# Performance work log

Measured on AMD Instinct MI355X. Metric: run time of the kernel, lower is better.

The kernel has to match this reference:

```python
import jax, jax.numpy as jnp
import numpy as np

LAM = 5.0
NUM_STEPS = 100
B, N, D = 8, 1024, 256


def setup_inputs() -> dict:
    key = jax.random.key(0)
    k1, k2 = jax.random.split(key)
    fA = jax.random.normal(k1, (B, N, D), dtype=jnp.float32)
    fB = jax.random.normal(k2, (B, N, D), dtype=jnp.float32)
    dustbin = jnp.zeros((1,), dtype=jnp.float32)  # learned dustbin score, init 0.0
    return {"fA": fA, "fB": fB, "dustbin": dustbin}


def _l2_normalize(x, eps=1e-12):
    # matches tf.math.l2_normalize: x / sqrt(max(sum(x^2), eps))
    return x * jax.lax.rsqrt(jnp.maximum(jnp.sum(x * x, axis=-1, keepdims=True), eps))


def _forward(fA, fB, dustbin):
    b, n, _ = fA.shape
    fA = _l2_normalize(fA)
    fB = _l2_normalize(fB)
    Sij = jnp.einsum('bnd,bmd->bnm', fA, fB)  # (B, N, N)
    # augment with dustbin row/col -> (B, N+1, N+1)
    row = dustbin * jnp.ones((b, 1, n), Sij.dtype)
    col = dustbin * jnp.ones((b, n + 1, 1), Sij.dtype)
    S_aug = jnp.concatenate([jnp.concatenate([Sij, row], axis=1), col], axis=2)
    Cij = jnp.clip(-S_aug, -15.0 / LAM, 15.0 / LAM)
    # marginals: [1,...,1, N] for both rows and cols
    ab = jnp.concatenate([jnp.ones((n,), Sij.dtype), jnp.full((1,), float(n), Sij.dtype)])[None, :]  # (1, N+1)
    P = jnp.exp(-LAM * Cij)
    P = P / jnp.sum(P, axis=(1, 2), keepdims=True)

    def step(P, _):
        # NOTE: row_sum/col_sum both computed from the SAME P, as in the TF code
        row_sum = jnp.sum(P, axis=1)  # (B, N+1)
        col_sum = jnp.sum(P, axis=2)  # (B, N+1)
        P = P * (ab / col_sum)[:, :, None]
        P = P * (ab / row_sum)[:, None, :]
        return P, None

    P, _ = jax.lax.scan(jax.checkpoint(step), P, None, length=NUM_STEPS)
    return P


def reference(fA, fB, dustbin):
    return _forward(fA, fB, dustbin)
```

## Files before the change

### kernel.cpp

```cpp
#include <hip/hip_runtime.h>
#include <math.h>
#include <stdint.h>

#define NB 8
#define NN 1024
#define DD 256
#define NP1 1025
#define LDP 1028
#define NSTEPS 100

__global__ __launch_bounds__(256) void norm_kernel(const float* __restrict__ fA,
                                                   const float* __restrict__ fB,
                                                   float* __restrict__ invA,
                                                   float* __restrict__ invB) {
  int gw = (blockIdx.x * 256 + threadIdx.x) >> 6;
  int lane = threadIdx.x & 63;
  const float* src;
  float* dst;
  int row;
  if (gw < NB * NN) { src = fA; dst = invA; row = gw; }
  else              { src = fB; dst = invB; row = gw - NB * NN; }
  float4 v = *(const float4*)(src + (size_t)row * DD + lane * 4);
  double ss = (double)v.x * v.x + (double)v.y * v.y + (double)v.z * v.z + (double)v.w * v.w;
#pragma unroll
  for (int o = 32; o; o >>= 1) ss += __shfl_xor(ss, o, 64);
  if (lane == 0) dst[row] = (float)(1.0 / sqrt(fmax(ss, 1e-12)));
}

__global__ __launch_bounds__(256) void gemm_exp_kernel(const float* __restrict__ fA,
                                                       const float* __restrict__ fB,
                                                       const float* __restrict__ invA,
                                                       const float* __restrict__ invB,
                                                       float* __restrict__ P0,
                                                       double* __restrict__ partZ) {
  const int id = blockIdx.x;
  const int b = id & 7;
  const int tile = id >> 3;
  const int bx = tile & 15, by = tile >> 4;
  const int row0 = by * 64, col0 = bx * 64;
  const int tid = threadIdx.x;
  const int tx = tid & 15, ty = tid >> 4;
  __shared__ __align__(16) float As[16][68];
  __shared__ __align__(16) float Bs[16][68];
  __shared__ double zred[256];
  float acc[4][4] = {{0.f}};
  const int lm = tid >> 2, kq = (tid & 3) << 2;
  const float sa = invA[b * NN + row0 + lm];
  const float sb = invB[b * NN + col0 + lm];
  const float* pA = fA + (size_t)(b * NN + row0 + lm) * DD + kq;
  const float* pB = fB + (size_t)(b * NN + col0 + lm) * DD + kq;
  for (int k0 = 0; k0 < DD; k0 += 16) {
    const float4 a4 = *(const float4*)(pA + k0);
    const float4 b4 = *(const float4*)(pB + k0);
    As[kq + 0][lm] = a4.x * sa; As[kq + 1][lm] = a4.y * sa;
    As[kq + 2][lm] = a4.z * sa; As[kq + 3][lm] = a4.w * sa;
    Bs[kq + 0][lm] = b4.x * sb; Bs[kq + 1][lm] = b4.y * sb;
    Bs[kq + 2][lm] = b4.z * sb; Bs[kq + 3][lm] = b4.w * sb;
    __syncthreads();
#pragma unroll
    for (int kk = 0; kk < 16; ++kk) {
      const float4 av = *(const float4*)&As[kk][ty * 4];
      const float4 bv = *(const float4*)&Bs[kk][tx * 4];
      const float ar[4] = {av.x, av.y, av.z, av.w};
      const float br[4] = {bv.x, bv.y, bv.z, bv.w};
#pragma unroll
      for (int a = 0; a < 4; ++a)
#pragma unroll
        for (int e = 0; e < 4; ++e)
          acc[a][e] = fmaf(ar[a], br[e], acc[a][e]);
    }
    __syncthreads();
  }
  double zs = 0.0;
#pragma unroll
  for (int a = 0; a < 4; ++a)
#pragma unroll
    for (int e = 0; e < 4; ++e) {
      const float S = acc[a][e];
      const float C = fminf(fmaxf(-S, -3.0f), 3.0f);
      const float p = expf(-5.0f * C);
      acc[a][e] = p;
      zs += (double)p;
    }
  {
    float* P0b = P0 + (size_t)b * NP1 * LDP;
#pragma unroll
    for (int a = 0; a < 4; ++a) {
      float4 v;
      v.x = acc[a][0]; v.y = acc[a][1]; v.z = acc[a][2]; v.w = acc[a][3];
      *(float4*)(P0b + (size_t)(row0 + ty * 4 + a) * LDP + col0 + tx * 4) = v;
    }
  }
  zred[tid] = zs;
  __syncthreads();
#pragma unroll
  for (int o = 128; o; o >>= 1) {
    if (tid < o) zred[tid] += zred[tid + o];
    __syncthreads();
  }
  if (tid == 0) partZ[(b * 16 + by) * 16 + bx] = zred[0];
}

__global__ __launch_bounds__(1024) void fill_dustbin_kernel(const float* __restrict__ dustbin,
                                                            float* __restrict__ P0) {
  const int b = blockIdx.x, tid = threadIdx.x;
  const float d = dustbin[0];
  const float dv = expf(-5.0f * fminf(fmaxf(-d, -3.0f), 3.0f));
  float* P0b = P0 + (size_t)b * NP1 * LDP;
  for (int j = tid; j < NP1; j += 1024) {
    P0b[(size_t)NN * LDP + j] = dv;
    P0b[(size_t)j * LDP + NN] = dv;
  }
}

__global__ __launch_bounds__(256) void init_rc_kernel(const double* __restrict__ partZ,
                                                      float* __restrict__ r0,
                                                      double* __restrict__ Binit,
                                                      double* __restrict__ Bzero) {
  const int b = blockIdx.x, tid = threadIdx.x;
  __shared__ double red[256];
  red[tid] = partZ[b * 256 + tid];
  __syncthreads();
#pragma unroll
  for (int o = 128; o; o >>= 1) {
    if (tid < o) red[tid] += red[tid + o];
    __syncthreads();
  }
  const double Z = red[0];
  const float rv = (float)(1.0 / Z);
  for (int i = tid; i < NP1; i += 256) {
    r0[b * NP1 + i] = rv;
    Binit[b * NP1 + i] = (i == NN) ? (double)NN : 1.0;
    Bzero[b * NP1 + i] = 0.0;
  }
}

__global__ __launch_bounds__(512, 4) void step_kernel(const float* __restrict__ P0,
                                                      const float* __restrict__ rin,
                                                      float* __restrict__ rout,
                                                      const double* __restrict__ Bprev,
                                                      double* __restrict__ Bacc,
                                                      double* __restrict__ Bzero) {
  const int id = blockIdx.x;
  const int b = id & 7;
  const int s = id >> 3;
  const int tid = threadIdx.x;
  const int lane = tid & 63;
  const int wv = tid >> 6;

  __shared__ __align__(16) double c_lds[NP1 + 3];
  __shared__ __align__(16) float part_lds[8][LDP];

  const float* P0b = P0 + (size_t)b * NP1 * LDP;
  const float* rv_in = rin + b * NP1;
  const int rowA = s * 16 + wv;
  const int rowB = rowA + 8;
  const bool special = (s == 63 && wv == 7);
  const float wA = rv_in[rowA];
  const float wB = rv_in[rowB];
  const float4* pA4 = (const float4*)(P0b + (size_t)rowA * LDP);
  const float4* pB4 = (const float4*)(P0b + (size_t)rowB * LDP);
  const float4* pC4 = (const float4*)(P0b + (size_t)NN * LDP);

  float4 a4[4], b4[4];
#pragma unroll
  for (int k = 0; k < 4; ++k) {
    a4[k] = pA4[lane + (k << 6)];
    b4[k] = pB4[lane + (k << 6)];
  }
  float aT = 0.f, bT = 0.f;
  if (lane == 0) {
    aT = ((const float*)pA4)[NN];
    bT = ((const float*)pB4)[NN];
  }
  float4 c4[4];
  float cT = 0.f, wC = 0.f;
  if (special) {
#pragma unroll
    for (int k = 0; k < 4; ++k) c4[k] = pC4[lane + (k << 6)];
    if (lane == 0) cT = ((const float*)pC4)[NN];
    wC = rv_in[NN];
  }

  if (tid < 17) {
    const int idx = id * 17 + tid;
    if (idx < NB * NP1) Bzero[idx] = 0.0;
  }
  const double* Bp = Bprev + b * NP1;
  for (int j = tid; j < NP1; j += 512)
    c_lds[j] = ((j == NN) ? (double)NN : 1.0) / Bp[j];
  __syncthreads();

  double dotA = 0.0, dotB = 0.0, dotC = 0.0;
  float4 part[4];
#pragma unroll
  for (int k = 0; k < 4; ++k) {
    const int j4 = lane + (k << 6);
    const double2 c01 = *(const double2*)&c_lds[4 * j4];
    const double2 c23 = *(const double2*)&c_lds[4 * j4 + 2];
    dotA += (double)a4[k].x * c01.x + (double)a4[k].y * c01.y +
            (double)a4[k].z * c23.x + (double)a4[k].w * c23.y;
    dotB += (double)b4[k].x * c01.x + (double)b4[k].y * c01.y +
            (double)b4[k].z * c23.x + (double)b4[k].w * c23.y;
    part[k].x = fmaf(wA, a4[k].x, wB * b4[k].x);
    part[k].y = fmaf(wA, a4[k].y, wB * b4[k].y);
    part[k].z = fmaf(wA, a4[k].z, wB * b4[k].z);
    part[k].w = fmaf(wA, a4[k].w, wB * b4[k].w);
    if (special) {
      dotC += (double)c4[k].x * c01.x + (double)c4[k].y * c01.y +
              (double)c4[k].z * c23.x + (double)c4[k].w * c23.y;
      part[k].x = fmaf(wC, c4[k].x, part[k].x);
      part[k].y = fmaf(wC, c4[k].y, part[k].y);
      part[k].z = fmaf(wC, c4[k].z, part[k].z);
      part[k].w = fmaf(wC, c4[k].w, part[k].w);
    }
  }
  float ptail = 0.f;
  if (lane == 0) {
    const double cN = c_lds[NN];
    dotA += (double)aT * cN;
    dotB += (double)bT * cN;
    ptail = wA * aT + wB * bT;
    if (special) { dotC += (double)cT * cN; ptail = fmaf(wC, cT, ptail); }
  }
#pragma unroll
  for (int o = 32; o; o >>= 1) {
    dotA += __shfl_xor(dotA, o, 64);
    dotB += __shfl_xor(dotB, o, 64);
  }
  if (special) {
#pragma unroll
    for (int o = 32; o; o >>= 1) dotC += __shfl_xor(dotC, o, 64);
  }
  if (lane == 0) {
    float* ro = rout + b * NP1;
    ro[rowA] = (float)(1.0 / dotA);
    ro[rowB] = (float)(1.0 / dotB);
    if (special) ro[NN] = (float)((double)NN / dotC);
  }
  {
    float4* pl4 = (float4*)&part_lds[wv][0];
#pragma unroll
    for (int k = 0; k < 4; ++k) pl4[lane + (k << 6)] = part[k];
    if (lane == 0) part_lds[wv][NN] = ptail;
  }
  __syncthreads();
  double* Ba = Bacc + b * NP1;
  for (int j = tid; j < NP1; j += 512) {
    const float s0 = ((part_lds[0][j] + part_lds[1][j]) + (part_lds[2][j] + part_lds[3][j])) +
                     ((part_lds[4][j] + part_lds[5][j]) + (part_lds[6][j] + part_lds[7][j]));
    atomicAdd(Ba + j, (double)s0);
  }
}

__global__ __launch_bounds__(256) void cfinal_kernel(const double* __restrict__ Bfin,
                                                     float* __restrict__ cfin) {
  const int b = blockIdx.x;
  for (int j = threadIdx.x; j < NP1; j += 256)
    cfin[b * LDP + j] = (float)(((j == NN) ? (double)NN : 1.0) / Bfin[b * NP1 + j]);
}

__global__ __launch_bounds__(256) void finalize_kernel(const float* __restrict__ P0,
                                                       float* __restrict__ Pout,
                                                       const float* __restrict__ rfin,
                                                       const float* __restrict__ cfin) {
  const int bi = blockIdx.x;
  const int b = bi & 7, i = bi >> 3;
  const int tid = threadIdx.x;
  const float rv = rfin[b * NP1 + i];
  const float4* src = (const float4*)(P0 + (size_t)b * NP1 * LDP + (size_t)i * LDP);
  const float4* cv = (const float4*)(cfin + b * LDP);
  float* dst = Pout + (size_t)b * NP1 * NP1 + (size_t)i * NP1;
  const float4 p = src[tid];
  const float4 c = cv[tid];
  dst[tid * 4 + 0] = rv * p.x * c.x;
  dst[tid * 4 + 1] = rv * p.y * c.y;
  dst[tid * 4 + 2] = rv * p.z * c.z;
  dst[tid * 4 + 3] = rv * p.w * c.w;
  if (tid == 0)
    dst[NN] = rv * ((const float*)src)[NN] * cfin[b * LDP + NN];
}

extern "C" void kernel_launch(void* const* d_in, const int* in_sizes, int n_in,
                              void* d_out, int out_size, void* d_ws, size_t ws_size,
                              hipStream_t stream) {
  const float* fA = (const float*)d_in[0];
  const float* fB = (const float*)d_in[1];
  const float* dustbin = (const float*)d_in[2];

  float* Pout = (float*)d_out;

  float* P0 = (float*)d_ws;
  float* rbuf = P0 + (size_t)NB * NP1 * LDP;
  float* cfin = rbuf + 2 * NB * NP1;
  double* Bbuf = (double*)(((uintptr_t)(cfin + NB * LDP) + 15) & ~(uintptr_t)15);
  double* partZ = Bbuf + 3 * NB * NP1;
  float* invA = (float*)(partZ + NB * 256);
  float* invB = invA + NB * NN;

  norm_kernel<<<4096, 256, 0, stream>>>(fA, fB, invA, invB);
  gemm_exp_kernel<<<2048, 256, 0, stream>>>(fA, fB, invA, invB, P0, partZ);
  fill_dustbin_kernel<<<NB, 1024, 0, stream>>>(dustbin, P0);
  init_rc_kernel<<<NB, 256, 0, stream>>>(partZ, rbuf, Bbuf + 2 * NB * NP1, Bbuf);

  for (int t = 0; t < NSTEPS; ++t) {
    float* rin = rbuf + (t & 1) * NB * NP1;
    float* rout = rbuf + ((t + 1) & 1) * NB * NP1;
    double* Bprev = Bbuf + ((t + 2) % 3) * NB * NP1;
    double* Bacc = Bbuf + (t % 3) * NB * NP1;
    double* Bzero = Bbuf + ((t + 1) % 3) * NB * NP1;
    step_kernel<<<512, 512, 0, stream>>>(P0, rin, rout, Bprev, Bacc, Bzero);
  }

  cfinal_kernel<<<NB, 256, 0, stream>>>(Bbuf, cfin);
  finalize_kernel<<<NB * NP1, 256, 0, stream>>>(P0, Pout, rbuf, cfin);
}
```

Before: 967.6 us.

## Replace per-step launches with a persistent cooperative Sinkhorn kernel caching P0 in LDS

```diff
diff --git a/kernel.cpp b/kernel.cpp
--- a/kernel.cpp
+++ b/kernel.cpp
@@ -113,10 +113,10 @@
   }
 }
 
-__global__ __launch_bounds__(256) void init_rc_kernel(const double* __restrict__ partZ,
-                                                      float* __restrict__ r0,
-                                                      double* __restrict__ Binit,
-                                                      double* __restrict__ Bzero) {
+__global__ __launch_bounds__(256) void init2_kernel(const double* __restrict__ partZ,
+                                                    float* __restrict__ rinit,
+                                                    double* __restrict__ B0,
+                                                    unsigned* __restrict__ ctr) {
   const int b = blockIdx.x, tid = threadIdx.x;
   __shared__ double red[256];
   red[tid] = partZ[b * 256 + tid];
@@ -126,131 +126,161 @@
     if (tid < o) red[tid] += red[tid + o];
     __syncthreads();
   }
-  const double Z = red[0];
-  const float rv = (float)(1.0 / Z);
-  for (int i = tid; i < NP1; i += 256) {
-    r0[b * NP1 + i] = rv;
-    Binit[b * NP1 + i] = (i == NN) ? (double)NN : 1.0;
-    Bzero[b * NP1 + i] = 0.0;
-  }
-}
-
-__global__ __launch_bounds__(512, 4) void step_kernel(const float* __restrict__ P0,
-                                                      const float* __restrict__ rin,
-                                                      float* __restrict__ rout,
-                                                      const double* __restrict__ Bprev,
-                                                      double* __restrict__ Bacc,
-                                                      double* __restrict__ Bzero) {
+  if (tid == 0) rinit[b] = (float)(1.0 / red[0]);
+  for (int j = tid; j < NP1; j += 256) B0[b * NP1 + j] = 0.0;
+  for (int t = tid; t < NSTEPS; t += 256) ctr[t * 8 + b] = 0u;
+}
+
+__global__ __launch_bounds__(512) void sinkhorn_persist(const float* __restrict__ P0,
+                                                        const float* __restrict__ dustbin,
+                                                        const float* __restrict__ rinit,
+                                                        double* __restrict__ Bbuf,
+                                                        unsigned* __restrict__ ctr,
+                                                        float* __restrict__ rfin) {
+  __shared__ __align__(16) float P0s[32][LDP];
+  __shared__ __align__(16) float c_f[LDP];
+  __shared__ __align__(16) float part[LDP];
+  __shared__ double wred[8];
+  __shared__ float rN_sh;
+
   const int id = blockIdx.x;
   const int b = id & 7;
   const int s = id >> 3;
   const int tid = threadIdx.x;
   const int lane = tid & 63;
   const int wv = tid >> 6;
-
-  __shared__ __align__(16) double c_lds[NP1 + 3];
-  __shared__ __align__(16) float part_lds[8][LDP];
-
-  const float* P0b = P0 + (size_t)b * NP1 * LDP;
-  const float* rv_in = rin + b * NP1;
-  const int rowA = s * 16 + wv;
-  const int rowB = rowA + 8;
-  const bool special = (s == 63 && wv == 7);
-  const float wA = rv_in[rowA];
-  const float wB = rv_in[rowB];
-  const float4* pA4 = (const float4*)(P0b + (size_t)rowA * LDP);
-  const float4* pB4 = (const float4*)(P0b + (size_t)rowB * LDP);
-  const float4* pC4 = (const float4*)(P0b + (size_t)NN * LDP);
-
-  float4 a4[4], b4[4];
-#pragma unroll
-  for (int k = 0; k < 4; ++k) {
-    a4[k] = pA4[lane + (k << 6)];
-    b4[k] = pB4[lane + (k << 6)];
-  }
-  float aT = 0.f, bT = 0.f;
+  const int row0 = s * 32;
+  const int wrow = wv * 4;
+  const bool desig = (s == 31);
+
+  const float d = dustbin[0];
+  const float dv = expf(-5.0f * fminf(fmaxf(-d, -3.0f), 3.0f));
+
+  {
+    const float4* src = (const float4*)(P0 + ((size_t)b * NP1 + row0) * LDP);
+    float4* dst = (float4*)&P0s[0][0];
+    for (int idx = tid; idx < 32 * (LDP / 4); idx += 512) dst[idx] = src[idx];
+  }
+  const float rv0 = rinit[b];
+  float r4[4] = {rv0, rv0, rv0, rv0};
+  if (tid == 0) rN_sh = rv0;
+  __syncthreads();
+
+  for (int t = 0; t < NSTEPS; ++t) {
+    double* Bacc = Bbuf + (size_t)(t % 3) * NB * NP1 + (size_t)b * NP1;
+    if (t == 0) {
+      for (int j = tid; j < LDP; j += 512) c_f[j] = 1.0f;
+    } else {
+      double* Bp = Bbuf + (size_t)((t + 2) % 3) * NB * NP1 + (size_t)b * NP1;
+      for (int j = tid; j < NP1; j += 512) {
+        const double bj = __hip_atomic_load(&Bp[j], __ATOMIC_RELAXED, __HIP_MEMORY_SCOPE_AGENT);
+        c_f[j] = (float)(((j == NN) ? (double)NN : 1.0) / bj);
+      }
+      if (tid < 3) c_f[NP1 + tid] = 0.0f;
+    }
+    {
+      double cs = (t == 0) ? ((tid == 0) ? 3.0 : 2.0)
+                           : (double)c_f[tid] + (double)c_f[tid + 512] +
+                             ((tid == 0) ? (double)c_f[1024] : 0.0);
+#pragma unroll
+      for (int o = 32; o; o >>= 1) cs += __shfl_xor(cs, o, 64);
+      if (lane == 0) wred[wv] = cs;
+    }
+    {
+      double* Bz = Bbuf + (size_t)((t + 1) % 3) * NB * NP1 + (size_t)b * NP1;
+      if (tid < 33) {
+        const int j = s * 33 + tid;
+        if (j < NP1) __hip_atomic_store(&Bz[j], 0.0, __ATOMIC_RELAXED, __HIP_MEMORY_SCOPE_AGENT);
+      }
+    }
+    {
+      const float pinit = desig ? rN_sh * dv : 0.0f;
+      for (int j = tid; j < LDP; j += 512) part[j] = pinit;
+    }
+    __syncthreads();
+
+    const float cN = c_f[NN];
+    double dot0 = 0.0, dot1 = 0.0, dot2 = 0.0, dot3 = 0.0;
+    float4 pacc[4];
+#pragma unroll
+    for (int k = 0; k < 4; ++k) { pacc[k].x = 0.f; pacc[k].y = 0.f; pacc[k].z = 0.f; pacc[k].w = 0.f; }
+#pragma unroll
+    for (int k = 0; k < 4; ++k) {
+      const int j4 = (lane << 2) + (k << 8);
+      const float4 cc = *(const float4*)&c_f[j4];
+      const double c0 = cc.x, c1 = cc.y, c2 = cc.z, c3 = cc.w;
+#pragma unroll
+      for (int q = 0; q < 4; ++q) {
+        const float4 v = *(const float4*)&P0s[wrow + q][j4];
+        const double dd = (double)v.x * c0 + (double)v.y * c1 +
+                          (double)v.z * c2 + (double)v.w * c3;
+        if (q == 0) dot0 += dd; else if (q == 1) dot1 += dd;
+        else if (q == 2) dot2 += dd; else dot3 += dd;
+        pacc[k].x = fmaf(r4[q], v.x, pacc[k].x);
+        pacc[k].y = fmaf(r4[q], v.y, pacc[k].y);
+        pacc[k].z = fmaf(r4[q], v.z, pacc[k].z);
+        pacc[k].w = fmaf(r4[q], v.w, pacc[k].w);
+      }
+    }
+    float ptail = 0.f;
+    if (lane == 0) {
+#pragma unroll
+      for (int q = 0; q < 4; ++q) {
+        const float vN = P0s[wrow + q][NN];
+        const double dd = (double)vN * (double)cN;
+        if (q == 0) dot0 += dd; else if (q == 1) dot1 += dd;
+        else if (q == 2) dot2 += dd; else dot3 += dd;
+        ptail = fmaf(r4[q], vN, ptail);
+      }
+    }
+#pragma unroll
+    for (int o = 32; o; o >>= 1) {
+      dot0 += __shfl_xor(dot0, o, 64);
+      dot1 += __shfl_xor(dot1, o, 64);
+      dot2 += __shfl_xor(dot2, o, 64);
+      dot3 += __shfl_xor(dot3, o, 64);
+    }
+    r4[0] = (float)(1.0 / dot0);
+    r4[1] = (float)(1.0 / dot1);
+    r4[2] = (float)(1.0 / dot2);
+    r4[3] = (float)(1.0 / dot3);
+#pragma unroll
+    for (int k = 0; k < 4; ++k) {
+      const int j4 = (lane << 2) + (k << 8);
+      atomicAdd(&part[j4 + 0], pacc[k].x);
+      atomicAdd(&part[j4 + 1], pacc[k].y);
+      atomicAdd(&part[j4 + 2], pacc[k].z);
+      atomicAdd(&part[j4 + 3], pacc[k].w);
+    }
+    if (lane == 0) atomicAdd(&part[NN], ptail);
+    if (desig && tid == 0) {
+      const double sumc = ((wred[0] + wred[1]) + (wred[2] + wred[3])) +
+                          ((wred[4] + wred[5]) + (wred[6] + wred[7]));
+      rN_sh = (float)((double)NN / ((double)dv * sumc));
+    }
+    __syncthreads();
+    for (int j = tid; j < NP1; j += 512)
+      atomicAdd(&Bacc[j], (double)part[j]);
+    if (t < NSTEPS - 1) {
+      __syncthreads();
+      if (tid == 0) {
+        __hip_atomic_fetch_add(&ctr[t * 8 + b], 1u, __ATOMIC_RELEASE, __HIP_MEMORY_SCOPE_AGENT);
+        unsigned v = 0; int guard = 0;
+        do {
+          v = __hip_atomic_load(&ctr[t * 8 + b], __ATOMIC_ACQUIRE, __HIP_MEMORY_SCOPE_AGENT);
+          if (v >= 32u) break;
+          __builtin_amdgcn_s_sleep(1);
+        } while (++guard < (1 << 20));
+      }
+      __syncthreads();
+    }
+  }
   if (lane == 0) {
-    aT = ((const float*)pA4)[NN];
-    bT = ((const float*)pB4)[NN];
-  }
-  float4 c4[4];
-  float cT = 0.f, wC = 0.f;
-  if (special) {
-#pragma unroll
-    for (int k = 0; k < 4; ++k) c4[k] = pC4[lane + (k << 6)];
-    if (lane == 0) cT = ((const float*)pC4)[NN];
-    wC = rv_in[NN];
-  }
-
-  if (tid < 17) {
-    const int idx = id * 17 + tid;
-    if (idx < NB * NP1) Bzero[idx] = 0.0;
-  }
-  const double* Bp = Bprev + b * NP1;
-  for (int j = tid; j < NP1; j += 512)
-    c_lds[j] = ((j == NN) ? (double)NN : 1.0) / Bp[j];
-  __syncthreads();
-
-  double dotA = 0.0, dotB = 0.0, dotC = 0.0;
-  float4 part[4];
-#pragma unroll
-  for (int k = 0; k < 4; ++k) {
-    const int j4 = lane + (k << 6);
-    const double2 c01 = *(const double2*)&c_lds[4 * j4];
-    const double2 c23 = *(const double2*)&c_lds[4 * j4 + 2];
-    dotA += (double)a4[k].x * c01.x + (double)a4[k].y * c01.y +
-            (double)a4[k].z * c23.x + (double)a4[k].w * c23.y;
-    dotB += (double)b4[k].x * c01.x + (double)b4[k].y * c01.y +
-            (double)b4[k].z * c23.x + (double)b4[k].w * c23.y;
-    part[k].x = fmaf(wA, a4[k].x, wB * b4[k].x);
-    part[k].y = fmaf(wA, a4[k].y, wB * b4[k].y);
-    part[k].z = fmaf(wA, a4[k].z, wB * b4[k].z);
-    part[k].w = fmaf(wA, a4[k].w, wB * b4[k].w);
-    if (special) {
-      dotC += (double)c4[k].x * c01.x + (double)c4[k].y * c01.y +
-              (double)c4[k].z * c23.x + (double)c4[k].w * c23.y;
-      part[k].x = fmaf(wC, c4[k].x, part[k].x);
-      part[k].y = fmaf(wC, c4[k].y, part[k].y);
-      part[k].z = fmaf(wC, c4[k].z, part[k].z);
-      part[k].w = fmaf(wC, c4[k].w, part[k].w);
-    }
-  }
-  float ptail = 0.f;
-  if (lane == 0) {
-    const double cN = c_lds[NN];
-    dotA += (double)aT * cN;
-    dotB += (double)bT * cN;
-    ptail = wA * aT + wB * bT;
-    if (special) { dotC += (double)cT * cN; ptail = fmaf(wC, cT, ptail); }
-  }
-#pragma unroll
-  for (int o = 32; o; o >>= 1) {
-    dotA += __shfl_xor(dotA, o, 64);
-    dotB += __shfl_xor(dotB, o, 64);
-  }
-  if (special) {
-#pragma unroll
-    for (int o = 32; o; o >>= 1) dotC += __shfl_xor(dotC, o, 64);
-  }
-  if (lane == 0) {
-    float* ro = rout + b * NP1;
-    ro[rowA] = (float)(1.0 / dotA);
-    ro[rowB] = (float)(1.0 / dotB);
-    if (special) ro[NN] = (float)((double)NN / dotC);
-  }
-  {
-    float4* pl4 = (float4*)&part_lds[wv][0];
-#pragma unroll
-    for (int k = 0; k < 4; ++k) pl4[lane + (k << 6)] = part[k];
-    if (lane == 0) part_lds[wv][NN] = ptail;
-  }
-  __syncthreads();
-  double* Ba = Bacc + b * NP1;
-  for (int j = tid; j < NP1; j += 512) {
-    const float s0 = ((part_lds[0][j] + part_lds[1][j]) + (part_lds[2][j] + part_lds[3][j])) +
-                     ((part_lds[4][j] + part_lds[5][j]) + (part_lds[6][j] + part_lds[7][j]));
-    atomicAdd(Ba + j, (double)s0);
-  }
+    float* ro = rfin + b * NP1;
+#pragma unroll
+    for (int q = 0; q < 4; ++q) ro[row0 + wrow + q] = r4[q];
+  }
+  if (desig && tid == 0) rfin[b * NP1 + NN] = rN_sh;
 }
 
 __global__ __launch_bounds__(256) void cfinal_kernel(const double* __restrict__ Bfin,
@@ -291,27 +321,25 @@
   float* Pout = (float*)d_out;
 
   float* P0 = (float*)d_ws;
-  float* rbuf = P0 + (size_t)NB * NP1 * LDP;
-  float* cfin = rbuf + 2 * NB * NP1;
+  float* rfin = P0 + (size_t)NB * NP1 * LDP;
+  float* cfin = rfin + NB * NP1;
   double* Bbuf = (double*)(((uintptr_t)(cfin + NB * LDP) + 15) & ~(uintptr_t)15);
   double* partZ = Bbuf + 3 * NB * NP1;
-  float* invA = (float*)(partZ + NB * 256);
+  float* rinit = (float*)(partZ + NB * 256);
+  unsigned* ctr = (unsigned*)(rinit + 8);
+  float* invA = (float*)(ctr + NSTEPS * 8);
   float* invB = invA + NB * NN;
 
   norm_kernel<<<4096, 256, 0, stream>>>(fA, fB, invA, invB);
   gemm_exp_kernel<<<2048, 256, 0, stream>>>(fA, fB, invA, invB, P0, partZ);
   fill_dustbin_kernel<<<NB, 1024, 0, stream>>>(dustbin, P0);
-  init_rc_kernel<<<NB, 256, 0, stream>>>(partZ, rbuf, Bbuf + 2 * NB * NP1, Bbuf);
-
-  for (int t = 0; t < NSTEPS; ++t) {
-    float* rin = rbuf + (t & 1) * NB * NP1;
-    float* rout = rbuf + ((t + 1) & 1) * NB * NP1;
-    double* Bprev = Bbuf + ((t + 2) % 3) * NB * NP1;
-    double* Bacc = Bbuf + (t % 3) * NB * NP1;
-    double* Bzero = Bbuf + ((t + 1) % 3) * NB * NP1;
-    step_kernel<<<512, 512, 0, stream>>>(P0, rin, rout, Bprev, Bacc, Bzero);
-  }
+  init2_kernel<<<NB, 256, 0, stream>>>(partZ, rinit, Bbuf, ctr);
+
+  void* args[] = {(void*)&P0, (void*)&dustbin, (void*)&rinit,
+                  (void*)&Bbuf, (void*)&ctr, (void*)&rfin};
+  hipLaunchCooperativeKernel((const void*)sinkhorn_persist, dim3(256), dim3(512),
+                             args, 0, stream);
 
   cfinal_kernel<<<NB, 256, 0, stream>>>(Bbuf, cfin);
-  finalize_kernel<<<NB * NP1, 256, 0, stream>>>(P0, Pout, rbuf, cfin);
-}
+  finalize_kernel<<<NB * NP1, 256, 0, stream>>>(P0, Pout, rfin, cfin);
+}
```

Result: slower. 2.174 ms (+124.7%).

## Store P0 as dense NxN and handle dustbin row/column analytically

Applied to the files above, without the earlier changes.

```diff
diff --git a/kernel.cpp b/kernel.cpp
--- a/kernel.cpp
+++ b/kernel.cpp
@@ -6,7 +6,7 @@
 #define NN 1024
 #define DD 256
 #define NP1 1025
-#define LDP 1028
+#define LDC 1028
 #define NSTEPS 100
 
 __global__ __launch_bounds__(256) void norm_kernel(const float* __restrict__ fA,
@@ -83,12 +83,12 @@
       zs += (double)p;
     }
   {
-    float* P0b = P0 + (size_t)b * NP1 * LDP;
+    float* P0b = P0 + (size_t)b * NN * NN;
 #pragma unroll
     for (int a = 0; a < 4; ++a) {
       float4 v;
       v.x = acc[a][0]; v.y = acc[a][1]; v.z = acc[a][2]; v.w = acc[a][3];
-      *(float4*)(P0b + (size_t)(row0 + ty * 4 + a) * LDP + col0 + tx * 4) = v;
+      *(float4*)(P0b + (size_t)(row0 + ty * 4 + a) * NN + col0 + tx * 4) = v;
     }
   }
   zred[tid] = zs;
@@ -99,18 +99,6 @@
     __syncthreads();
   }
   if (tid == 0) partZ[(b * 16 + by) * 16 + bx] = zred[0];
-}
-
-__global__ __launch_bounds__(1024) void fill_dustbin_kernel(const float* __restrict__ dustbin,
-                                                            float* __restrict__ P0) {
-  const int b = blockIdx.x, tid = threadIdx.x;
-  const float d = dustbin[0];
-  const float dv = expf(-5.0f * fminf(fmaxf(-d, -3.0f), 3.0f));
-  float* P0b = P0 + (size_t)b * NP1 * LDP;
-  for (int j = tid; j < NP1; j += 1024) {
-    P0b[(size_t)NN * LDP + j] = dv;
-    P0b[(size_t)j * LDP + NN] = dv;
-  }
 }
 
 __global__ __launch_bounds__(256) void init_rc_kernel(const double* __restrict__ partZ,
@@ -136,6 +124,7 @@
 }
 
 __global__ __launch_bounds__(512, 4) void step_kernel(const float* __restrict__ P0,
+                                                      const float* __restrict__ dustbin,
                                                       const float* __restrict__ rin,
                                                       float* __restrict__ rout,
                                                       const double* __restrict__ Bprev,
@@ -147,20 +136,26 @@
   const int tid = threadIdx.x;
   const int lane = tid & 63;
   const int wv = tid >> 6;
-
-  __shared__ __align__(16) double c_lds[NP1 + 3];
-  __shared__ __align__(16) float part_lds[8][LDP];
-
-  const float* P0b = P0 + (size_t)b * NP1 * LDP;
+  const bool desig = (s == 63);
+
+  __shared__ __align__(16) float c_f[NN];
+  __shared__ __align__(16) float part_lds[8][NN];
+  __shared__ double wredR[8];
+  __shared__ double wredC[8];
+  __shared__ double cN_sh;
+
+  const float d = dustbin[0];
+  const float dv = expf(-5.0f * fminf(fmaxf(-d, -3.0f), 3.0f));
+  const double dv_d = (double)dv;
+
+  const float* P0b = P0 + (size_t)b * NN * NN;
   const float* rv_in = rin + b * NP1;
   const int rowA = s * 16 + wv;
   const int rowB = rowA + 8;
-  const bool special = (s == 63 && wv == 7);
   const float wA = rv_in[rowA];
   const float wB = rv_in[rowB];
-  const float4* pA4 = (const float4*)(P0b + (size_t)rowA * LDP);
-  const float4* pB4 = (const float4*)(P0b + (size_t)rowB * LDP);
-  const float4* pC4 = (const float4*)(P0b + (size_t)NN * LDP);
+  const float4* pA4 = (const float4*)(P0b + (size_t)rowA * NN);
+  const float4* pB4 = (const float4*)(P0b + (size_t)rowB * NN);
 
   float4 a4[4], b4[4];
 #pragma unroll
@@ -168,88 +163,77 @@
     a4[k] = pA4[lane + (k << 6)];
     b4[k] = pB4[lane + (k << 6)];
   }
-  float aT = 0.f, bT = 0.f;
-  if (lane == 0) {
-    aT = ((const float*)pA4)[NN];
-    bT = ((const float*)pB4)[NN];
-  }
-  float4 c4[4];
-  float cT = 0.f, wC = 0.f;
-  if (special) {
-#pragma unroll
-    for (int k = 0; k < 4; ++k) c4[k] = pC4[lane + (k << 6)];
-    if (lane == 0) cT = ((const float*)pC4)[NN];
-    wC = rv_in[NN];
-  }
 
   if (tid < 17) {
     const int idx = id * 17 + tid;
     if (idx < NB * NP1) Bzero[idx] = 0.0;
   }
   const double* Bp = Bprev + b * NP1;
-  for (int j = tid; j < NP1; j += 512)
-    c_lds[j] = ((j == NN) ? (double)NN : 1.0) / Bp[j];
+  for (int j = tid; j < NN; j += 512) c_f[j] = (float)(1.0 / Bp[j]);
+  if (tid == 0) cN_sh = (double)NN / Bp[NN];
   __syncthreads();
-
-  double dotA = 0.0, dotB = 0.0, dotC = 0.0;
-  float4 part[4];
+  const double cN = cN_sh;
+
+  double dotA = 0.0, dotB = 0.0;
+  float4 pk[4];
 #pragma unroll
   for (int k = 0; k < 4; ++k) {
     const int j4 = lane + (k << 6);
-    const double2 c01 = *(const double2*)&c_lds[4 * j4];
-    const double2 c23 = *(const double2*)&c_lds[4 * j4 + 2];
-    dotA += (double)a4[k].x * c01.x + (double)a4[k].y * c01.y +
-            (double)a4[k].z * c23.x + (double)a4[k].w * c23.y;
-    dotB += (double)b4[k].x * c01.x + (double)b4[k].y * c01.y +
-            (double)b4[k].z * c23.x + (double)b4[k].w * c23.y;
-    part[k].x = fmaf(wA, a4[k].x, wB * b4[k].x);
-    part[k].y = fmaf(wA, a4[k].y, wB * b4[k].y);
-    part[k].z = fmaf(wA, a4[k].z, wB * b4[k].z);
-    part[k].w = fmaf(wA, a4[k].w, wB * b4[k].w);
-    if (special) {
-      dotC += (double)c4[k].x * c01.x + (double)c4[k].y * c01.y +
-              (double)c4[k].z * c23.x + (double)c4[k].w * c23.y;
-      part[k].x = fmaf(wC, c4[k].x, part[k].x);
-      part[k].y = fmaf(wC, c4[k].y, part[k].y);
-      part[k].z = fmaf(wC, c4[k].z, part[k].z);
-      part[k].w = fmaf(wC, c4[k].w, part[k].w);
-    }
-  }
-  float ptail = 0.f;
-  if (lane == 0) {
-    const double cN = c_lds[NN];
-    dotA += (double)aT * cN;
-    dotB += (double)bT * cN;
-    ptail = wA * aT + wB * bT;
-    if (special) { dotC += (double)cT * cN; ptail = fmaf(wC, cT, ptail); }
+    const float4 cc = ((const float4*)c_f)[j4];
+    dotA += (double)a4[k].x * (double)cc.x + (double)a4[k].y * (double)cc.y +
+            (double)a4[k].z * (double)cc.z + (double)a4[k].w * (double)cc.w;
+    dotB += (double)b4[k].x * (double)cc.x + (double)b4[k].y * (double)cc.y +
+            (double)b4[k].z * (double)cc.z + (double)b4[k].w * (double)cc.w;
+    pk[k].x = fmaf(wA, a4[k].x, wB * b4[k].x);
+    pk[k].y = fmaf(wA, a4[k].y, wB * b4[k].y);
+    pk[k].z = fmaf(wA, a4[k].z, wB * b4[k].z);
+    pk[k].w = fmaf(wA, a4[k].w, wB * b4[k].w);
   }
 #pragma unroll
   for (int o = 32; o; o >>= 1) {
     dotA += __shfl_xor(dotA, o, 64);
     dotB += __shfl_xor(dotB, o, 64);
   }
-  if (special) {
-#pragma unroll
-    for (int o = 32; o; o >>= 1) dotC += __shfl_xor(dotC, o, 64);
-  }
+  dotA += dv_d * cN;
+  dotB += dv_d * cN;
   if (lane == 0) {
     float* ro = rout + b * NP1;
     ro[rowA] = (float)(1.0 / dotA);
     ro[rowB] = (float)(1.0 / dotB);
-    if (special) ro[NN] = (float)((double)NN / dotC);
+    wredR[wv] = (double)wA + (double)wB;
   }
   {
     float4* pl4 = (float4*)&part_lds[wv][0];
 #pragma unroll
-    for (int k = 0; k < 4; ++k) pl4[lane + (k << 6)] = part[k];
-    if (lane == 0) part_lds[wv][NN] = ptail;
+    for (int k = 0; k < 4; ++k) pl4[lane + (k << 6)] = pk[k];
+  }
+  {
+    double cs = (double)c_f[tid] + (double)c_f[tid + 512];
+#pragma unroll
+    for (int o = 32; o; o >>= 1) cs += __shfl_xor(cs, o, 64);
+    if (lane == 0) wredC[wv] = cs;
   }
   __syncthreads();
+
+  const float rN = rv_in[NN];
+  const float rNdv = rN * dv;
   double* Ba = Bacc + b * NP1;
-  for (int j = tid; j < NP1; j += 512) {
-    const float s0 = ((part_lds[0][j] + part_lds[1][j]) + (part_lds[2][j] + part_lds[3][j])) +
-                     ((part_lds[4][j] + part_lds[5][j]) + (part_lds[6][j] + part_lds[7][j]));
+  for (int j = tid; j < NN; j += 512) {
+    float s0 = ((part_lds[0][j] + part_lds[1][j]) + (part_lds[2][j] + part_lds[3][j])) +
+               ((part_lds[4][j] + part_lds[5][j]) + (part_lds[6][j] + part_lds[7][j]));
+    if (desig) s0 += rNdv;
     atomicAdd(Ba + j, (double)s0);
+  }
+  if (tid == 0) {
+    double rsum = ((wredR[0] + wredR[1]) + (wredR[2] + wredR[3])) +
+                  ((wredR[4] + wredR[5]) + (wredR[6] + wredR[7]));
+    if (desig) rsum += (double)rN;
+    atomicAdd(Ba + NN, dv_d * rsum);
+    if (desig) {
+      const double sc = ((wredC[0] + wredC[1]) + (wredC[2] + wredC[3])) +
+                        ((wredC[4] + wredC[5]) + (wredC[6] + wredC[7])) + cN;
+      rout[b * NP1 + NN] = (float)((double)NN / (dv_d * sc));
+    }
   }
 }
 
@@ -257,28 +241,39 @@
                                                      float* __restrict__ cfin) {
   const int b = blockIdx.x;
   for (int j = threadIdx.x; j < NP1; j += 256)
-    cfin[b * LDP + j] = (float)(((j == NN) ? (double)NN : 1.0) / Bfin[b * NP1 + j]);
+    cfin[b * LDC + j] = (float)(((j == NN) ? (double)NN : 1.0) / Bfin[b * NP1 + j]);
 }
 
 __global__ __launch_bounds__(256) void finalize_kernel(const float* __restrict__ P0,
+                                                       const float* __restrict__ dustbin,
                                                        float* __restrict__ Pout,
                                                        const float* __restrict__ rfin,
                                                        const float* __restrict__ cfin) {
   const int bi = blockIdx.x;
   const int b = bi & 7, i = bi >> 3;
   const int tid = threadIdx.x;
-  const float rv = rfin[b * NP1 + i];
-  const float4* src = (const float4*)(P0 + (size_t)b * NP1 * LDP + (size_t)i * LDP);
-  const float4* cv = (const float4*)(cfin + b * LDP);
+  const float d = dustbin[0];
+  const float dv = expf(-5.0f * fminf(fmaxf(-d, -3.0f), 3.0f));
+  const float4* cv = (const float4*)(cfin + b * LDC);
+  const float cN = cfin[b * LDC + NN];
   float* dst = Pout + (size_t)b * NP1 * NP1 + (size_t)i * NP1;
-  const float4 p = src[tid];
   const float4 c = cv[tid];
-  dst[tid * 4 + 0] = rv * p.x * c.x;
-  dst[tid * 4 + 1] = rv * p.y * c.y;
-  dst[tid * 4 + 2] = rv * p.z * c.z;
-  dst[tid * 4 + 3] = rv * p.w * c.w;
-  if (tid == 0)
-    dst[NN] = rv * ((const float*)src)[NN] * cfin[b * LDP + NN];
+  if (i < NN) {
+    const float rv = rfin[b * NP1 + i];
+    const float4 p = ((const float4*)(P0 + ((size_t)b * NN + i) * NN))[tid];
+    dst[tid * 4 + 0] = rv * p.x * c.x;
+    dst[tid * 4 + 1] = rv * p.y * c.y;
+    dst[tid * 4 + 2] = rv * p.z * c.z;
+    dst[tid * 4 + 3] = rv * p.w * c.w;
+    if (tid == 0) dst[NN] = rv * dv * cN;
+  } else {
+    const float rv = rfin[b * NP1 + NN];
+    dst[tid * 4 + 0] = rv * dv * c.x;
+    dst[tid * 4 + 1] = rv * dv * c.y;
+    dst[tid * 4 + 2] = rv * dv * c.z;
+    dst[tid * 4 + 3] = rv * dv * c.w;
+    if (tid == 0) dst[NN] = rv * dv * cN;
+  }
 }
 
 extern "C" void kernel_launch(void* const* d_in, const int* in_sizes, int n_in,
@@ -291,16 +286,15 @@
   float* Pout = (float*)d_out;
 
   float* P0 = (float*)d_ws;
-  float* rbuf = P0 + (size_t)NB * NP1 * LDP;
+  float* rbuf = P0 + (size_t)NB * NN * NN;
   float* cfin = rbuf + 2 * NB * NP1;
-  double* Bbuf = (double*)(((uintptr_t)(cfin + NB * LDP) + 15) & ~(uintptr_t)15);
+  double* Bbuf = (double*)(((uintptr_t)(cfin + NB * LDC) + 15) & ~(uintptr_t)15);
   double* partZ = Bbuf + 3 * NB * NP1;
   float* invA = (float*)(partZ + NB * 256);
   float* invB = invA + NB * NN;
 
   norm_kernel<<<4096, 256, 0, stream>>>(fA, fB, invA, invB);
   gemm_exp_kernel<<<2048, 256, 0, stream>>>(fA, fB, invA, invB, P0, partZ);
-  fill_dustbin_kernel<<<NB, 1024, 0, stream>>>(dustbin, P0);
   init_rc_kernel<<<NB, 256, 0, stream>>>(partZ, rbuf, Bbuf + 2 * NB * NP1, Bbuf);
 
   for (int t = 0; t < NSTEPS; ++t) {
@@ -309,9 +303,9 @@
     double* Bprev = Bbuf + ((t + 2) % 3) * NB * NP1;
     double* Bacc = Bbuf + (t % 3) * NB * NP1;
     double* Bzero = Bbuf + ((t + 1) % 3) * NB * NP1;
-    step_kernel<<<512, 512, 0, stream>>>(P0, rin, rout, Bprev, Bacc, Bzero);
+    step_kernel<<<512, 512, 0, stream>>>(P0, dustbin, rin, rout, Bprev, Bacc, Bzero);
   }
 
   cfinal_kernel<<<NB, 256, 0, stream>>>(Bbuf, cfin);
-  finalize_kernel<<<NB * NP1, 256, 0, stream>>>(P0, Pout, rbuf, cfin);
-}
+  finalize_kernel<<<NB * NP1, 256, 0, stream>>>(P0, dustbin, Pout, rbuf, cfin);
+}
```

Result: slower. 994.0 us (+2.7%).
